# Optimization experiments

Measured on AMD Instinct MI355X. Metric: run time of the kernel, lower is better.

The kernel has to match this reference:

```python
import math
import jax, jax.numpy as jnp
import numpy as np


def setup_inputs() -> dict:
    key = jax.random.key(0)
    k0, k1, k2 = jax.random.split(key, 3)
    b, c, h, w = 4, 256, 64, 64
    x = jax.random.normal(k0, (b, c, h, w), dtype=jnp.float32)
    # 1x1 conv weights stored as [out_ch, in_ch]
    qkv_w = jax.random.normal(k1, (3 * c, c), dtype=jnp.float32) / math.sqrt(c)
    qkv_b = jnp.zeros((3 * c,), dtype=jnp.float32)
    out_w = jax.random.normal(k2, (c, c), dtype=jnp.float32) / math.sqrt(c)
    out_b = jnp.zeros((c,), dtype=jnp.float32)
    return {"x": x, "qkv_w": qkv_w, "qkv_b": qkv_b, "out_w": out_w, "out_b": out_b}


def reference(x, qkv_w, qkv_b, out_w, out_b):
    b, c, h, w = x.shape
    n = h * w
    # 1x1 conv QKV projection: [b, 3c, h, w]
    qkv = jnp.einsum('oc,bchw->bohw', qkv_w, x) + qkv_b[None, :, None, None]
    # chunk along channels into q, k, v each [b, c, n]
    qkv = qkv.reshape(b, 3, c, n)
    q, k, v = qkv[:, 0], qkv[:, 1], qkv[:, 2]
    # attn[b, i, j] = sum_c k[b,c,i] * q[b,c,j] / sqrt(c); softmax over key axis (dim=-2 -> axis=1)
    scores = jnp.einsum('bcn,bcm->bnm', k, q) / math.sqrt(c)
    attn = jax.nn.softmax(scores, axis=1)
    # out[b, c, j] = sum_i v[b,c,i] * attn[b,i,j]
    o = jnp.einsum('bcn,bnm->bcm', v, attn).reshape(b, c, h, w)
    # output 1x1 conv
    return jnp.einsum('oc,bchw->bohw', out_w, o) + out_b[None, :, None, None]
```

## Files before the change

kernel.cpp:

```cpp
#include <hip/hip_runtime.h>
#include <hip/hip_bf16.h>

typedef unsigned short u16;
typedef unsigned int u32;
typedef __attribute__((ext_vector_type(8))) short short8;
typedef __attribute__((ext_vector_type(4))) short short4v;
typedef __attribute__((ext_vector_type(16))) float f32x16;

#define MFMA32 __builtin_amdgcn_mfma_f32_32x32x16_bf16

#define NSEQ 4096
#define CD 256
#define CF 0.09016844005556021f

__device__ __forceinline__ u16 f2bf(float f) {
  u32 u = __float_as_uint(f);
  u += 0x7fffu + ((u >> 16) & 1u);
  return (u16)(u >> 16);
}
__device__ __forceinline__ float bf2f(short s) {
  return __uint_as_float(((u32)(u16)s) << 16);
}
__device__ __forceinline__ u32 pk2bf(float a, float b) {
  union {
    __hip_bfloat162 h;
    u32 u;
  } cv;
  cv.h = __float22bfloat162_rn(make_float2(a, b));
  return cv.u;
}
__device__ __forceinline__ void async16(const void* g, void* l) {
  __builtin_amdgcn_global_load_lds(
      (const __attribute__((address_space(1))) u32*)g,
      (__attribute__((address_space(3))) u32*)l, 16, 0, 0);
}

__global__ void cast_w(const float* __restrict__ qkv_w,
                       const float* __restrict__ out_w, u16* __restrict__ wq,
                       u16* __restrict__ wo) {
  int idx = blockIdx.x * 256 + threadIdx.x;
  if (idx < 768 * CD) wq[idx] = f2bf(qkv_w[idx]);
  if (idx < CD * CD) wo[idx] = f2bf(out_w[idx]);
}

__global__ __launch_bounds__(256) void xpose(const float* __restrict__ x,
                                             u16* __restrict__ x_t) {
  __shared__ float tile[64][65];
  const int t = threadIdx.x;
  const int b = blockIdx.z;
  const int n0 = blockIdx.x * 64, c0 = blockIdx.y * 64;
  const float* xb = x + (size_t)b * CD * NSEQ;
  const int cr = t >> 4, nc4 = (t & 15) * 4;
#pragma unroll
  for (int i = 0; i < 4; ++i) {
    int c = cr + 16 * i;
    float4 v = *(const float4*)(xb + (size_t)(c0 + c) * NSEQ + n0 + nc4);
    tile[c][nc4 + 0] = v.x;
    tile[c][nc4 + 1] = v.y;
    tile[c][nc4 + 2] = v.z;
    tile[c][nc4 + 3] = v.w;
  }
  __syncthreads();
  const int n = t & 63, cc = (t >> 6) * 16;
  u16* dst = x_t + (size_t)b * NSEQ * CD + (size_t)(n0 + n) * CD + c0 + cc;
#pragma unroll
  for (int j = 0; j < 4; ++j) {
    short4v pv;
#pragma unroll
    for (int r = 0; r < 4; ++r) pv[r] = (short)f2bf(tile[cc + 4 * j + r][n]);
    *(short4v*)(dst + 4 * j) = pv;
  }
}

__global__ __launch_bounds__(512, 1) void qkv_gemm3(
    const u16* __restrict__ wq, const float* __restrict__ qkv_b,
    const u16* __restrict__ x_t, u16* __restrict__ q_t, u16* __restrict__ k_t,
    u16* __restrict__ v_) {
  __shared__ u16 __align__(16) Wls[128 * 256];
  __shared__ u16 __align__(16) Bls[128 * 256];
  const int t = threadIdx.x, w = t >> 6, lane = t & 63;
  const int l31 = lane & 31, l5 = lane >> 5;
  const int os = w & 3, nh = w >> 2;
  const int n0 = blockIdx.x * 128, o0 = blockIdx.y * 128, b = blockIdx.z;
  const u16* Xb = x_t + (size_t)b * NSEQ * CD;
#pragma unroll
  for (int j = 0; j < 8; ++j) {
    int r = w * 16 + j * 2 + l5;
    async16(wq + (size_t)(o0 + r) * CD + ((l31 ^ (r & 7)) * 8),
            Wls + (w * 16 + j * 2) * 256);
    async16(Xb + (size_t)(n0 + r) * CD + ((l31 ^ (r & 7)) * 8),
            Bls + (w * 16 + j * 2) * 256);
  }
  __builtin_amdgcn_s_waitcnt(0);
  __syncthreads();
  f32x16 acc0, acc1;
#pragma unroll
  for (int i = 0; i < 16; ++i) {
    acc0[i] = 0.f;
    acc1[i] = 0.f;
  }
  const int ra = os * 32 + l31;
  const int rb0 = nh * 64 + l31, rb1 = rb0 + 32;
#pragma unroll
  for (int kc = 0; kc < 16; ++kc) {
    short8 a = *(const short8*)(Wls + ra * 256 + (((kc * 2 + l5) ^ (ra & 7)) * 8));
    short8 b0 = *(const short8*)(Bls + rb0 * 256 + (((kc * 2 + l5) ^ (rb0 & 7)) * 8));
    short8 b1 = *(const short8*)(Bls + rb1 * 256 + (((kc * 2 + l5) ^ (rb1 & 7)) * 8));
    acc0 = MFMA32(a, b0, acc0, 0, 0, 0);
    acc1 = MFMA32(a, b1, acc1, 0, 0, 0);
  }
  const int otype = blockIdx.y >> 1;
  const int obase = o0 + os * 32;
#pragma unroll
  for (int na = 0; na < 2; ++na) {
    f32x16& acc = na ? acc1 : acc0;
    const int n_g = n0 + nh * 64 + na * 32 + l31;
    if (otype < 2) {
      u16* dst = (otype == 0 ? q_t : k_t) + (size_t)b * NSEQ * CD +
                 (size_t)n_g * CD + (obase - otype * 256);
#pragma unroll
      for (int g = 0; g < 4; ++g) {
        float4 bv = *(const float4*)(qkv_b + obase + g * 8 + l5 * 4);
        const float* bp = (const float*)&bv;
        short4v pk;
#pragma unroll
        for (int r = 0; r < 4; ++r) pk[r] = (short)f2bf(acc[g * 4 + r] + bp[r]);
        *(short4v*)(dst + g * 8 + l5 * 4) = pk;
      }
    } else {
      u16* dst = v_ + (size_t)b * CD * NSEQ;
#pragma unroll
      for (int g = 0; g < 4; ++g) {
        float4 bv = *(const float4*)(qkv_b + obase + g * 8 + l5 * 4);
        const float* bp = (const float*)&bv;
#pragma unroll
        for (int r = 0; r < 4; ++r) {
          int c = obase - 512 + g * 8 + l5 * 4 + r;
          dst[(size_t)c * NSEQ + n_g] = f2bf(acc[g * 4 + r] + bp[r]);
        }
      }
    }
  }
}

__global__ __launch_bounds__(512, 2) void flash7(const u16* __restrict__ q_t,
                                                 const u16* __restrict__ k_t,
                                                 const u16* __restrict__ v_,
                                                 u16* __restrict__ opart,
                                                 float2* __restrict__ ml) {
  __shared__ u16 __align__(16) Kls[2][64 * 256];
  __shared__ u16 __align__(16) Vls[2][256 * 64];

  const int t = threadIdx.x, w = t >> 6, lane = t & 63;
  const int l31 = lane & 31, l5 = lane >> 5;
  const int s = w >> 1, nh = w & 1;

  const int linear = blockIdx.x;
  const int xcd = linear & 7, slot = linear >> 3;
  const int b = xcd >> 1, half = xcd & 1;
  const int m0 = slot * 128;
  const int nbase = half * 2048;
  const int sid = half * 2 + nh;

  const u16* Qb = q_t + (size_t)b * NSEQ * CD;
  const u16* Kb = k_t + (size_t)b * NSEQ * CD;
  const u16* Vb = v_ + (size_t)b * CD * NSEQ;

  const int mrow = m0 + s * 32 + l31;

  short8 qf[16];
#pragma unroll
  for (int kc = 0; kc < 16; ++kc)
    qf[kc] = *(const short8*)(Qb + (size_t)mrow * CD + kc * 16 + l5 * 8);

  const int kr = w * 8;
  const int vrb = w * 32;
  const int vr_lane = lane >> 3, vc_lane = lane & 7;

#pragma unroll
  for (int j = 0; j < 4; ++j) {
    int r = kr + j * 2 + l5;
    async16(Kb + (size_t)(nbase + r) * CD + ((l31 ^ (r & 7)) * 8),
            &Kls[0][(kr + j * 2) * 256]);
    int rv = vrb + j * 8 + vr_lane;
    async16(Vb + (size_t)rv * NSEQ + nbase + ((vc_lane ^ (rv & 7)) * 8),
            &Vls[0][(vrb + j * 8) * 64]);
  }

  float mst = -3.0e38f, lst = 0.f;
  f32x16 oa[8];
#pragma unroll
  for (int i = 0; i < 8; ++i)
#pragma unroll
    for (int r = 0; r < 16; ++r) oa[i][r] = 0.f;

  for (int tt = 0; tt < 32; ++tt) {
    const int cur = tt & 1;
    __builtin_amdgcn_s_waitcnt(0);
    __syncthreads();
    if (tt + 1 < 32) {
      const int n0 = nbase + (tt + 1) * 64;
      const int nxt = cur ^ 1;
#pragma unroll
      for (int j = 0; j < 4; ++j) {
        int r = kr + j * 2 + l5;
        async16(Kb + (size_t)(n0 + r) * CD + ((l31 ^ (r & 7)) * 8),
                &Kls[nxt][(kr + j * 2) * 256]);
        int rv = vrb + j * 8 + vr_lane;
        async16(Vb + (size_t)rv * NSEQ + n0 + ((vc_lane ^ (rv & 7)) * 8),
                &Vls[nxt][(vrb + j * 8) * 64]);
      }
    }
    f32x16 sa;
#pragma unroll
    for (int i = 0; i < 16; ++i) sa[i] = 0.f;
    const int rk = nh * 32 + l31;
#pragma unroll
    for (int kc = 0; kc < 16; ++kc) {
      short8 a =
          *(const short8*)(&Kls[cur][rk * 256 + (((kc * 2 + l5) ^ (rk & 7)) * 8)]);
      sa = MFMA32(a, qf[kc], sa, 0, 0, 0);
    }
    float rm = sa[0];
#pragma unroll
    for (int i = 1; i < 16; ++i) rm = fmaxf(rm, sa[i]);
    rm = fmaxf(rm, __shfl_xor(rm, 32));
    float mnew = fmaxf(mst, rm * CF);
    float al = exp2f(mst - mnew);
    mst = mnew;
    u32 d[4][2];
    float ls = 0.f;
#pragma unroll
    for (int gg = 0; gg < 4; ++gg) {
      float p0 = exp2f(sa[gg * 4 + 0] * CF - mnew);
      float p1 = exp2f(sa[gg * 4 + 1] * CF - mnew);
      float p2 = exp2f(sa[gg * 4 + 2] * CF - mnew);
      float p3 = exp2f(sa[gg * 4 + 3] * CF - mnew);
      ls += (p0 + p1) + (p2 + p3);
      d[gg][0] = pk2bf(p0, p1);
      d[gg][1] = pk2bf(p2, p3);
    }
    ls += __shfl_xor(ls, 32);
    lst = lst * al + ls;
    if (__ballot(al != 1.0f)) {
#pragma unroll
      for (int i = 0; i < 8; ++i)
#pragma unroll
        for (int r = 0; r < 16; ++r) oa[i][r] *= al;
    }
    short8 pf[2];
#pragma unroll
    for (int f = 0; f < 2; ++f) {
      const int g0 = f * 2;
      u32 sx0 = l5 ? d[g0][0] : d[g0 + 1][0];
      u32 sx1 = l5 ? d[g0][1] : d[g0 + 1][1];
      u32 e0 = (u32)__shfl_xor((int)sx0, 32);
      u32 e1 = (u32)__shfl_xor((int)sx1, 32);
      union {
        u32 u[4];
        short8 s8;
      } cv;
      cv.u[0] = l5 ? e0 : d[g0][0];
      cv.u[1] = l5 ? e1 : d[g0][1];
      cv.u[2] = l5 ? d[g0 + 1][0] : e0;
      cv.u[3] = l5 ? d[g0 + 1][1] : e1;
      pf[f] = cv.s8;
    }
#pragma unroll
    for (int f = 0; f < 2; ++f) {
#pragma unroll
      for (int ct = 0; ct < 8; ++ct) {
        int c = ct * 32 + l31;
        short8 vf = *(const short8*)(&Vls[cur][c * 64 +
                                               (((nh * 4 + f * 2 + l5) ^ (c & 7)) * 8)]);
        oa[ct] = MFMA32(vf, pf[f], oa[ct], 0, 0, 0);
      }
    }
  }

  float inv = 1.0f / lst;
  u16* dst = opart + ((size_t)(sid * 4 + b) * NSEQ + mrow) * CD;
#pragma unroll
  for (int ct = 0; ct < 8; ++ct)
#pragma unroll
    for (int gg = 0; gg < 4; ++gg) {
      short4v pk;
#pragma unroll
      for (int r = 0; r < 4; ++r) pk[r] = (short)f2bf(oa[ct][gg * 4 + r] * inv);
      *(short4v*)(dst + ct * 32 + gg * 8 + l5 * 4) = pk;
    }
  if (lane < 32)
    ml[(size_t)(sid * 4 + b) * NSEQ + mrow] = make_float2(mst, lst);
}

__global__ __launch_bounds__(512, 1) void out_gemm6(
    const u16* __restrict__ wo, const float* __restrict__ out_b,
    const u16* __restrict__ opart, const float2* __restrict__ ml,
    float* __restrict__ out) {
  __shared__ u16 __align__(16) Wls[128 * 256];
  __shared__ u16 __align__(16) Bls[128 * 256];
  const int t = threadIdx.x, w = t >> 6, lane = t & 63;
  const int l31 = lane & 31, l5 = lane >> 5;
  const int os = w & 3, nh = w >> 2;
  const int n0 = blockIdx.x * 128, o0 = blockIdx.y * 128, b = blockIdx.z;
#pragma unroll
  for (int j = 0; j < 8; ++j) {
    int r = w * 16 + j * 2 + l5;
    async16(wo + (size_t)(o0 + r) * CD + ((l31 ^ (r & 7)) * 8),
            Wls + (w * 16 + j * 2) * 256);
  }
#pragma unroll
  for (int i = 0; i < 8; ++i) {
    int idx = i * 512 + t;
    int r = idx >> 5, p = idx & 31;
    int n = n0 + r;
    float2 st[4];
#pragma unroll
    for (int q = 0; q < 4; ++q) st[q] = ml[(size_t)(q * 4 + b) * NSEQ + n];
    float M = fmaxf(fmaxf(st[0].x, st[1].x), fmaxf(st[2].x, st[3].x));
    float wt[4], tot = 0.f;
#pragma unroll
    for (int q = 0; q < 4; ++q) {
      wt[q] = st[q].y * exp2f(st[q].x - M);
      tot += wt[q];
    }
    float inv = 1.0f / tot;
    float acc[8] = {};
#pragma unroll
    for (int q = 0; q < 4; ++q) {
      float wq_ = wt[q] * inv;
      short8 xq =
          *(const short8*)(opart + ((size_t)(q * 4 + b) * NSEQ + n) * CD + p * 8);
#pragma unroll
      for (int e = 0; e < 8; ++e) acc[e] += wq_ * bf2f(xq[e]);
    }
    short8 om;
#pragma unroll
    for (int e = 0; e < 8; ++e) om[e] = (short)f2bf(acc[e]);
    *(short8*)(Bls + r * 256 + ((p ^ (r & 7)) * 8)) = om;
  }
  __builtin_amdgcn_s_waitcnt(0);
  __syncthreads();
  f32x16 acc0, acc1;
#pragma unroll
  for (int i = 0; i < 16; ++i) {
    acc0[i] = 0.f;
    acc1[i] = 0.f;
  }
  const int ra = os * 32 + l31;
  const int rb0 = nh * 64 + l31, rb1 = rb0 + 32;
#pragma unroll
  for (int kc = 0; kc < 16; ++kc) {
    short8 a = *(const short8*)(Wls + ra * 256 + (((kc * 2 + l5) ^ (ra & 7)) * 8));
    short8 b0 = *(const short8*)(Bls + rb0 * 256 + (((kc * 2 + l5) ^ (rb0 & 7)) * 8));
    short8 b1 = *(const short8*)(Bls + rb1 * 256 + (((kc * 2 + l5) ^ (rb1 & 7)) * 8));
    acc0 = MFMA32(a, b0, acc0, 0, 0, 0);
    acc1 = MFMA32(a, b1, acc1, 0, 0, 0);
  }
  const int obase = o0 + os * 32;
#pragma unroll
  for (int na = 0; na < 2; ++na) {
    f32x16& acc = na ? acc1 : acc0;
    const int n_g = n0 + nh * 64 + na * 32 + l31;
#pragma unroll
    for (int g = 0; g < 4; ++g) {
      float4 bv = *(const float4*)(out_b + obase + g * 8 + l5 * 4);
      const float* bp = (const float*)&bv;
#pragma unroll
      for (int r = 0; r < 4; ++r) {
        int o = obase + g * 8 + l5 * 4 + r;
        out[((size_t)b * CD + o) * NSEQ + n_g] = acc[g * 4 + r] + bp[r];
      }
    }
  }
}

extern "C" void kernel_launch(void* const* d_in, const int* in_sizes, int n_in,
                              void* d_out, int out_size, void* d_ws,
                              size_t ws_size, hipStream_t stream) {
  const float* x = (const float*)d_in[0];
  const float* qkv_w = (const float*)d_in[1];
  const float* qkv_b = (const float*)d_in[2];
  const float* out_w = (const float*)d_in[3];
  const float* out_b = (const float*)d_in[4];
  float* out = (float*)d_out;

  const size_t SZ = (size_t)4 * NSEQ * CD;
  u16* x_t = (u16*)d_ws;
  u16* q_t = x_t + SZ;
  u16* k_t = q_t + SZ;
  u16* v_ = k_t + SZ;
  u16* opart = v_ + SZ;
  u16* wq = opart + 4 * SZ;
  u16* wo = wq + 768 * CD;
  float2* ml = (float2*)(wo + CD * CD);

  cast_w<<<dim3(768), dim3(256), 0, stream>>>(qkv_w, out_w, wq, wo);
  xpose<<<dim3(64, 4, 4), dim3(256), 0, stream>>>(x, x_t);
  qkv_gemm3<<<dim3(32, 6, 4), dim3(512), 0, stream>>>(wq, qkv_b, x_t, q_t, k_t,
                                                      v_);
  flash7<<<dim3(256), dim3(512), 0, stream>>>(q_t, k_t, v_, opart, ml);
  out_gemm6<<<dim3(32, 2, 4), dim3(512), 0, stream>>>(wo, out_b, opart, ml,
                                                      out);
}
```

Before: 230.3 us.

## Split flash attention into 4-wave blocks with 32-key tiles and fuse weight cast

The flash kernel moves from 512-thread blocks (128 query rows times 2 key halves split across waves) to 256-thread blocks, each owning 128 query rows and a quarter of the keys, iterating over 32-key tiles. Shared K/V buffers shrink and the V tile uses a new swizzled layout. This doubles the grid and halves LDS per block, so more blocks can be resident and the split-K partitions get finer. The weight bf16 cast is folded into the transpose kernel to save a launch. In exchange each block issues a barrier and a smaller async load per 32-key step, so synchronisation cost per unit of work goes up.

After: 206.4 us. 1.12x faster.

```diff
diff --git a/kernel.cpp b/kernel.cpp
--- a/kernel.cpp
+++ b/kernel.cpp
@@ -35,18 +35,22 @@
       (__attribute__((address_space(3))) u32*)l, 16, 0, 0);
 }
 
-__global__ void cast_w(const float* __restrict__ qkv_w,
-                       const float* __restrict__ out_w, u16* __restrict__ wq,
-                       u16* __restrict__ wo) {
-  int idx = blockIdx.x * 256 + threadIdx.x;
-  if (idx < 768 * CD) wq[idx] = f2bf(qkv_w[idx]);
-  if (idx < CD * CD) wo[idx] = f2bf(out_w[idx]);
-}
-
-__global__ __launch_bounds__(256) void xpose(const float* __restrict__ x,
-                                             u16* __restrict__ x_t) {
+__global__ __launch_bounds__(256) void xpose_cast(const float* __restrict__ x,
+                                                  u16* __restrict__ x_t,
+                                                  const float* __restrict__ qkv_w,
+                                                  const float* __restrict__ out_w,
+                                                  u16* __restrict__ wq,
+                                                  u16* __restrict__ wo) {
   __shared__ float tile[64][65];
   const int t = threadIdx.x;
+  {
+    int lin = blockIdx.x + 64 * (blockIdx.y + 4 * blockIdx.z);
+    int widx = lin * 256 + t;
+    if (widx < 768 * CD)
+      wq[widx] = f2bf(qkv_w[widx]);
+    else
+      wo[widx - 768 * CD] = f2bf(out_w[widx - 768 * CD]);
+  }
   const int b = blockIdx.z;
   const int n0 = blockIdx.x * 64, c0 = blockIdx.y * 64;
   const float* xb = x + (size_t)b * CD * NSEQ;
@@ -143,48 +147,56 @@
   }
 }
 
-__global__ __launch_bounds__(512, 2) void flash7(const u16* __restrict__ q_t,
+__global__ __launch_bounds__(256, 2) void flash8(const u16* __restrict__ q_t,
                                                  const u16* __restrict__ k_t,
                                                  const u16* __restrict__ v_,
                                                  u16* __restrict__ opart,
                                                  float2* __restrict__ ml) {
-  __shared__ u16 __align__(16) Kls[2][64 * 256];
-  __shared__ u16 __align__(16) Vls[2][256 * 64];
+  __shared__ u16 __align__(16) Kls[2][32 * 256];
+  __shared__ u16 __align__(16) Vls[2][128 * 64];
 
   const int t = threadIdx.x, w = t >> 6, lane = t & 63;
   const int l31 = lane & 31, l5 = lane >> 5;
-  const int s = w >> 1, nh = w & 1;
 
   const int linear = blockIdx.x;
   const int xcd = linear & 7, slot = linear >> 3;
-  const int b = xcd >> 1, half = xcd & 1;
-  const int m0 = slot * 128;
-  const int nbase = half * 2048;
-  const int sid = half * 2 + nh;
+  const int b = xcd >> 1;
+  const int q = (xcd & 1) * 2 + (slot >> 5);
+  const int mblk = slot & 31;
+  const int m0 = mblk * 128;
+  const int nbase = q * 1024;
 
   const u16* Qb = q_t + (size_t)b * NSEQ * CD;
   const u16* Kb = k_t + (size_t)b * NSEQ * CD;
   const u16* Vb = v_ + (size_t)b * CD * NSEQ;
 
-  const int mrow = m0 + s * 32 + l31;
+  const int mrow = m0 + w * 32 + l31;
 
   short8 qf[16];
 #pragma unroll
   for (int kc = 0; kc < 16; ++kc)
     qf[kc] = *(const short8*)(Qb + (size_t)mrow * CD + kc * 16 + l5 * 8);
 
-  const int kr = w * 8;
-  const int vrb = w * 32;
-  const int vr_lane = lane >> 3, vc_lane = lane & 7;
-
+  int krow[4];
+  const u16* ksrc[4];
 #pragma unroll
   for (int j = 0; j < 4; ++j) {
-    int r = kr + j * 2 + l5;
-    async16(Kb + (size_t)(nbase + r) * CD + ((l31 ^ (r & 7)) * 8),
-            &Kls[0][(kr + j * 2) * 256]);
-    int rv = vrb + j * 8 + vr_lane;
-    async16(Vb + (size_t)rv * NSEQ + nbase + ((vc_lane ^ (rv & 7)) * 8),
-            &Vls[0][(vrb + j * 8) * 64]);
+    krow[j] = w * 8 + j * 2 + l5;
+    ksrc[j] = Kb + (size_t)krow[j] * CD + ((l31 ^ (krow[j] & 7)) * 8);
+  }
+  const u16* vsrc[4];
+#pragma unroll
+  for (int j = 0; j < 4; ++j) {
+    int c2 = w * 32 + j * 8 + (lane >> 3);
+    int chl = (lane & 7) ^ (c2 & 7);
+    int c = (c2 << 1) | (chl >> 2);
+    vsrc[j] = Vb + (size_t)c * NSEQ + (chl & 3) * 8;
+  }
+
+#pragma unroll
+  for (int j = 0; j < 4; ++j) {
+    async16(ksrc[j] + (size_t)nbase * CD, &Kls[0][(w * 8 + j * 2) * 256]);
+    async16(vsrc[j] + nbase, &Vls[0][(w * 32 + j * 8) * 64]);
   }
 
   float mst = -3.0e38f, lst = 0.f;
@@ -199,26 +211,21 @@
     __builtin_amdgcn_s_waitcnt(0);
     __syncthreads();
     if (tt + 1 < 32) {
-      const int n0 = nbase + (tt + 1) * 64;
+      const int n0 = nbase + (tt + 1) * 32;
       const int nxt = cur ^ 1;
 #pragma unroll
       for (int j = 0; j < 4; ++j) {
-        int r = kr + j * 2 + l5;
-        async16(Kb + (size_t)(n0 + r) * CD + ((l31 ^ (r & 7)) * 8),
-                &Kls[nxt][(kr + j * 2) * 256]);
-        int rv = vrb + j * 8 + vr_lane;
-        async16(Vb + (size_t)rv * NSEQ + n0 + ((vc_lane ^ (rv & 7)) * 8),
-                &Vls[nxt][(vrb + j * 8) * 64]);
+        async16(ksrc[j] + (size_t)n0 * CD, &Kls[nxt][(w * 8 + j * 2) * 256]);
+        async16(vsrc[j] + n0, &Vls[nxt][(w * 32 + j * 8) * 64]);
       }
     }
     f32x16 sa;
 #pragma unroll
     for (int i = 0; i < 16; ++i) sa[i] = 0.f;
-    const int rk = nh * 32 + l31;
 #pragma unroll
     for (int kc = 0; kc < 16; ++kc) {
       short8 a =
-          *(const short8*)(&Kls[cur][rk * 256 + (((kc * 2 + l5) ^ (rk & 7)) * 8)]);
+          *(const short8*)(&Kls[cur][l31 * 256 + (((kc * 2 + l5) ^ (l31 & 7)) * 8)]);
       sa = MFMA32(a, qf[kc], sa, 0, 0, 0);
     }
     float rm = sa[0];
@@ -270,16 +277,17 @@
     for (int f = 0; f < 2; ++f) {
 #pragma unroll
       for (int ct = 0; ct < 8; ++ct) {
-        int c = ct * 32 + l31;
-        short8 vf = *(const short8*)(&Vls[cur][c * 64 +
-                                               (((nh * 4 + f * 2 + l5) ^ (c & 7)) * 8)]);
+        int c2r = ct * 16 + (l31 >> 1);
+        int chl = ((l31 & 1) << 2) | (f * 2 + l5);
+        short8 vf =
+            *(const short8*)(&Vls[cur][c2r * 64 + ((chl ^ (c2r & 7)) * 8)]);
         oa[ct] = MFMA32(vf, pf[f], oa[ct], 0, 0, 0);
       }
     }
   }
 
   float inv = 1.0f / lst;
-  u16* dst = opart + ((size_t)(sid * 4 + b) * NSEQ + mrow) * CD;
+  u16* dst = opart + ((size_t)(q * 4 + b) * NSEQ + mrow) * CD;
 #pragma unroll
   for (int ct = 0; ct < 8; ++ct)
 #pragma unroll
@@ -290,7 +298,7 @@
       *(short4v*)(dst + ct * 32 + gg * 8 + l5 * 4) = pk;
     }
   if (lane < 32)
-    ml[(size_t)(sid * 4 + b) * NSEQ + mrow] = make_float2(mst, lst);
+    ml[(size_t)(q * 4 + b) * NSEQ + mrow] = make_float2(mst, lst);
 }
 
 __global__ __launch_bounds__(512, 1) void out_gemm6(
@@ -316,21 +324,21 @@
     int n = n0 + r;
     float2 st[4];
 #pragma unroll
-    for (int q = 0; q < 4; ++q) st[q] = ml[(size_t)(q * 4 + b) * NSEQ + n];
+    for (int qq = 0; qq < 4; ++qq) st[qq] = ml[(size_t)(qq * 4 + b) * NSEQ + n];
     float M = fmaxf(fmaxf(st[0].x, st[1].x), fmaxf(st[2].x, st[3].x));
     float wt[4], tot = 0.f;
 #pragma unroll
-    for (int q = 0; q < 4; ++q) {
-      wt[q] = st[q].y * exp2f(st[q].x - M);
-      tot += wt[q];
+    for (int qq = 0; qq < 4; ++qq) {
+      wt[qq] = st[qq].y * exp2f(st[qq].x - M);
+      tot += wt[qq];
     }
     float inv = 1.0f / tot;
     float acc[8] = {};
 #pragma unroll
-    for (int q = 0; q < 4; ++q) {
-      float wq_ = wt[q] * inv;
+    for (int qq = 0; qq < 4; ++qq) {
+      float wq_ = wt[qq] * inv;
       short8 xq =
-          *(const short8*)(opart + ((size_t)(q * 4 + b) * NSEQ + n) * CD + p * 8);
+          *(const short8*)(opart + ((size_t)(qq * 4 + b) * NSEQ + n) * CD + p * 8);
 #pragma unroll
       for (int e = 0; e < 8; ++e) acc[e] += wq_ * bf2f(xq[e]);
     }
@@ -395,11 +403,11 @@
   u16* wo = wq + 768 * CD;
   float2* ml = (float2*)(wo + CD * CD);
 
-  cast_w<<<dim3(768), dim3(256), 0, stream>>>(qkv_w, out_w, wq, wo);
-  xpose<<<dim3(64, 4, 4), dim3(256), 0, stream>>>(x, x_t);
+  xpose_cast<<<dim3(64, 4, 4), dim3(256), 0, stream>>>(x, x_t, qkv_w, out_w,
+                                                       wq, wo);
   qkv_gemm3<<<dim3(32, 6, 4), dim3(512), 0, stream>>>(wq, qkv_b, x_t, q_t, k_t,
                                                       v_);
-  flash7<<<dim3(256), dim3(512), 0, stream>>>(q_t, k_t, v_, opart, ml);
+  flash8<<<dim3(512), dim3(256), 0, stream>>>(q_t, k_t, v_, opart, ml);
   out_gemm6<<<dim3(32, 2, 4), dim3(512), 0, stream>>>(wo, out_b, opart, ml,
                                                       out);
 }
```
